# Performance work log

Measured on AMD Instinct MI355X. Metric: run time of the kernel, lower is better.

The kernel has to match this reference:

```python
import jax, jax.numpy as jnp
import numpy as np

N = 5          # ngram order
N_SYM = 64     # alphabet size
D = N_SYM * (N - 1)
B, L = 32, 4096


def setup_inputs() -> dict:
    key = jax.random.key(0)
    kx, kw, kb = jax.random.split(key, 3)
    x = jax.random.randint(kx, (B, L), 0, N_SYM, dtype=jnp.int64)
    # nn.Linear(D, N_sym): W is (N_sym, D), b is (N_sym,)
    bound = 1.0 / np.sqrt(D)
    W = jax.random.uniform(kw, (N_SYM, D), jnp.float32, -bound, bound)
    b = jax.random.uniform(kb, (N_SYM,), jnp.float32, -bound, bound)
    return {"x": x, "W": W, "b": b}


def _encode(x):
    # ngram at output position j covers x[:, j-n+1 : j] (length n-1, excludes j)
    # windows: (B, L-(n-1), n-1)
    win = jnp.stack([x[:, p : L - (N - 1) + p] for p in range(N - 1)], axis=-1)
    oh = jax.nn.one_hot(win, N_SYM, dtype=jnp.float32)  # (B, L', n-1, N_sym)
    # torch flattens enc[(sym, pos)] row-major -> feature = sym*(n-1)+pos
    oh = jnp.transpose(oh, (0, 1, 3, 2)).reshape(B, L - (N - 1), D)
    # positions j < n-1 are all-zero rows
    return jnp.pad(oh, ((0, 0), (N - 1, 0), (0, 0)))  # (B, L, D)


def reference(x, W, b):
    enc = _encode(x)                                   # (B, L, D)
    logits = jnp.einsum('bld,vd->blv', enc, W) + b     # (B, L, N_sym)
    return logits
```

## Files before the change

### kernel.cpp

```cpp
#include <hip/hip_runtime.h>


#define NSYM   64
#define CTX    4
#define DFEAT  256
#define LSEQ   4096
#define NPOS   (32 * LSEQ)
#define IPW    16
#define WAVES  4
#define POS_PER_BLOCK (WAVES * 64)
#define BLOCKS (NPOS / POS_PER_BLOCK)

typedef float vfloat4 __attribute__((ext_vector_type(4)));

static __device__ __forceinline__ unsigned f2bf(float f) {
    unsigned u = __float_as_uint(f);
    return (u + 0x7fffu + ((u >> 16) & 1u)) >> 16;
}

__global__ __launch_bounds__(256, 2)
void loglinear_kernel(const int* __restrict__ x,
                      const float* __restrict__ W,
                      const float* __restrict__ bias,
                      float* __restrict__ out) {
    __shared__ unsigned int wt[DFEAT * 32];
    __shared__ int          xs[POS_PER_BLOCK + CTX];

    const int t  = threadIdx.x;
    const int PB = blockIdx.x * POS_PER_BLOCK;
    const int jb = PB & (LSEQ - 1);

    for (int k = t; k < POS_PER_BLOCK + CTX; k += 256) {
        xs[k] = (jb == 0 && k < CTX) ? 0 : x[PB - CTX + k];
    }

    {
        const int vp    = t & 31;
        const int chunk = t >> 5;
        const int q = vp >> 1, h = vp & 1;
        #pragma unroll
        for (int it = 0; it < 8; ++it) {
            const int d0 = (chunk * 8 + it) * 4;
            const float4 a = *reinterpret_cast<const float4*>(W + (2*vp)     * DFEAT + d0);
            const float4 b = *reinterpret_cast<const float4*>(W + (2*vp + 1) * DFEAT + d0);
            const float av[4] = {a.x, a.y, a.z, a.w};
            const float bv[4] = {b.x, b.y, b.z, b.w};
            #pragma unroll
            for (int k = 0; k < 4; ++k) {
                const int d = d0 + k;
                wt[d*32 + ((((q + d) & 15) << 1) + h)] = f2bf(av[k]) | (f2bf(bv[k]) << 16);
            }
        }
    }
    __syncthreads();

    const int lane = t & 63;
    const int wave = t >> 6;
    const int g = lane >> 4;
    const int q = lane & 15;

    const float4 bq = reinterpret_cast<const float4*>(bias)[q];
    const vfloat4 b4 = {bq.x, bq.y, bq.z, bq.w};

    const int jbase = wave * 64;
    vfloat4* __restrict__ out4 = reinterpret_cast<vfloat4*>(out);
    const size_t outbase = (size_t)PB * 16 + q;

    #pragma unroll
    for (int ii = 0; ii < IPW; ++ii) {
        const int jloc = jbase + ii * 4 + g;
        vfloat4 acc = b4;
        if (jb + jloc >= CTX) {
            #pragma unroll
            for (int p = 0; p < CTX; ++p) {
                const int c = xs[jloc + p] * 4 + p;
                const uint2 wp = *reinterpret_cast<const uint2*>(
                    &wt[c * 32 + (((q + c) & 15) << 1)]);
                acc.x += __uint_as_float(wp.x << 16);
                acc.y += __uint_as_float(wp.x & 0xffff0000u);
                acc.z += __uint_as_float(wp.y << 16);
                acc.w += __uint_as_float(wp.y & 0xffff0000u);
            }
        }
        out4[outbase + (size_t)jloc * 16] = acc;
    }
}

extern "C" void kernel_launch(void* const* d_in, const int* in_sizes, int n_in,
                              void* d_out, int out_size, void* d_ws, size_t ws_size,
                              hipStream_t stream) {
    const int*   x   = (const int*)d_in[0];
    const float* W   = (const float*)d_in[1];
    const float* b   = (const float*)d_in[2];
    float*       out = (float*)d_out;

    hipLaunchKernelGGL(loglinear_kernel, dim3(BLOCKS), dim3(256), 0, stream,
                       x, W, b, out);
}
```

Baseline: 16.62 us.

## Keep W in fp32 LDS, pack context symbols per position, drop bf16 conversion

Stores the weight table in shared memory as fp32, transposed to a [feature][vocab] layout, instead of packed and swizzled bf16 pairs. Each position's four context symbols are packed into one 32-bit word, so the inner loop does one LDS read for the context plus one float4 read and add per symbol. This removes the bf16 rounding and unpacking work and the swizzle arithmetic, and improves accuracy. In exchange it doubles LDS use to 64KB per block, which may limit the 2 blocks per CU occupancy target, and the new 128-bit LDS reads may hit bank conflicts.

After: 15.43 us. -7.2%, faster.

```diff
diff --git a/kernel.cpp b/kernel.cpp
--- a/kernel.cpp
+++ b/kernel.cpp
@@ -7,49 +7,45 @@
 #define LSEQ   4096
 #define NPOS   (32 * LSEQ)
 #define IPW    16
-#define WAVES  4
-#define POS_PER_BLOCK (WAVES * 64)
+#define POS_PER_BLOCK 256
 #define BLOCKS (NPOS / POS_PER_BLOCK)
 
 typedef float vfloat4 __attribute__((ext_vector_type(4)));
-
-static __device__ __forceinline__ unsigned f2bf(float f) {
-    unsigned u = __float_as_uint(f);
-    return (u + 0x7fffu + ((u >> 16) & 1u)) >> 16;
-}
 
 __global__ __launch_bounds__(256, 2)
 void loglinear_kernel(const int* __restrict__ x,
                       const float* __restrict__ W,
                       const float* __restrict__ bias,
                       float* __restrict__ out) {
-    __shared__ unsigned int wt[DFEAT * 32];
-    __shared__ int          xs[POS_PER_BLOCK + CTX];
+    __shared__ float    wt[DFEAT * NSYM];
+    __shared__ unsigned xw[POS_PER_BLOCK];
 
     const int t  = threadIdx.x;
     const int PB = blockIdx.x * POS_PER_BLOCK;
     const int jb = PB & (LSEQ - 1);
 
-    for (int k = t; k < POS_PER_BLOCK + CTX; k += 256) {
-        xs[k] = (jb == 0 && k < CTX) ? 0 : x[PB - CTX + k];
+    {
+        unsigned w = 0;
+        #pragma unroll
+        for (int p = 0; p < CTX; ++p) {
+            const int idx = PB - CTX + t + p;
+            const int sym = (idx >= 0) ? x[idx] : 0;
+            w |= (unsigned)sym << (8 * p);
+        }
+        xw[t] = w;
     }
 
     {
-        const int vp    = t & 31;
-        const int chunk = t >> 5;
-        const int q = vp >> 1, h = vp & 1;
+        const int v = t & 63;
+        const int chunk = t >> 6;
         #pragma unroll
-        for (int it = 0; it < 8; ++it) {
-            const int d0 = (chunk * 8 + it) * 4;
-            const float4 a = *reinterpret_cast<const float4*>(W + (2*vp)     * DFEAT + d0);
-            const float4 b = *reinterpret_cast<const float4*>(W + (2*vp + 1) * DFEAT + d0);
-            const float av[4] = {a.x, a.y, a.z, a.w};
-            const float bv[4] = {b.x, b.y, b.z, b.w};
-            #pragma unroll
-            for (int k = 0; k < 4; ++k) {
-                const int d = d0 + k;
-                wt[d*32 + ((((q + d) & 15) << 1) + h)] = f2bf(av[k]) | (f2bf(bv[k]) << 16);
-            }
+        for (int it = 0; it < 16; ++it) {
+            const int d0 = (chunk * 16 + it) * 4;
+            const float4 wv = *reinterpret_cast<const float4*>(W + v * DFEAT + d0);
+            wt[(d0    ) * 64 + v] = wv.x;
+            wt[(d0 + 1) * 64 + v] = wv.y;
+            wt[(d0 + 2) * 64 + v] = wv.z;
+            wt[(d0 + 3) * 64 + v] = wv.w;
         }
     }
     __syncthreads();
@@ -63,26 +59,24 @@
     const vfloat4 b4 = {bq.x, bq.y, bq.z, bq.w};
 
     const int jbase = wave * 64;
-    vfloat4* __restrict__ out4 = reinterpret_cast<vfloat4*>(out);
-    const size_t outbase = (size_t)PB * 16 + q;
+    vfloat4* __restrict__ outp =
+        reinterpret_cast<vfloat4*>(out) + (size_t)(PB + jbase) * 16 + q;
 
     #pragma unroll
     for (int ii = 0; ii < IPW; ++ii) {
         const int jloc = jbase + ii * 4 + g;
+        const unsigned w = xw[jloc];
         vfloat4 acc = b4;
         if (jb + jloc >= CTX) {
             #pragma unroll
             for (int p = 0; p < CTX; ++p) {
-                const int c = xs[jloc + p] * 4 + p;
-                const uint2 wp = *reinterpret_cast<const uint2*>(
-                    &wt[c * 32 + (((q + c) & 15) << 1)]);
-                acc.x += __uint_as_float(wp.x << 16);
-                acc.y += __uint_as_float(wp.x & 0xffff0000u);
-                acc.z += __uint_as_float(wp.y << 16);
-                acc.w += __uint_as_float(wp.y & 0xffff0000u);
+                const int sym = (w >> (8 * p)) & 0xff;
+                const vfloat4 wv = *reinterpret_cast<const vfloat4*>(
+                    wt + sym * 256 + p * 64 + q * 4);
+                acc += wv;
             }
         }
-        out4[outbase + (size_t)jloc * 16] = acc;
+        outp[(ii * 4 + g) * 16] = acc;
     }
 }
 
```
